# Kernel tuning notes

Measured on AMD Instinct MI355X. Metric: run time of the kernel, lower is better.

## Reference

```python
import jax, jax.numpy as jnp
import numpy as np

BLOCK = 128
SPARSE_BLOCK = 128
SF = 4
NEG = jnp.finfo(jnp.float32).min


def _unfold(x, size, step):
    # x: (..., T, d) -> (..., b, size, d) overlapping windows (torch unfold + transpose)
    b = (x.shape[-2] - size) // step + 1
    idx = np.arange(b)[:, None] * step + np.arange(size)
    return x[..., idx, :]


def _pad_tokens(x, s, pad_value):
    cfg = [(0, 0)] * (x.ndim - 2) + [(s, s), (0, 0)]
    return jnp.pad(x, cfg, constant_values=pad_value)


def _local_blocks(x, pad_value):
    size, step = BLOCK * 3, BLOCK
    s = (size - step) // 2
    return _unfold(_pad_tokens(x, s, pad_value), size, step)


def _sparse_blocks(x, pad_value):
    size0, step = SPARSE_BLOCK * 3, BLOCK // SF
    odd = step % 2
    size = size0 * 2
    s = (size - step) // 2 + odd
    xw = _unfold(_pad_tokens(x, s, pad_value), size, step)
    if odd:
        xw = xw[..., :-1, :, :]
    u = (size - BLOCK * 3 // SF) // 2 + odd
    sb = SPARSE_BLOCK
    u_ = u + odd
    return jnp.concatenate([xw[..., u - sb:u, :], xw[..., -u_:-u_ + sb, :]], axis=-2)


def _cat_gsl(x_global, x_sparse, x_local):
    # x_local: (n,h,b,t_loc,d); broadcast global over block axis
    b = x_local.shape[-3]
    g = jnp.broadcast_to(x_global[..., None, :, :],
                         x_global.shape[:-2] + (b,) + x_global.shape[-2:])
    return jnp.concatenate([g, x_sparse, x_local], axis=-2)


def _build_lsg(x, x_sparse, x_global, pad_value):
    loc = _local_blocks(x, pad_value)
    sp = _sparse_blocks(x_sparse, pad_value)
    return _cat_gsl(x_global, sp, loc)


def reference(query_layer, key_layer, value_layer, attention_mask,
              sparse_key, sparse_value, sparse_mask,
              global_key, global_value, global_mask):
    n, h, t, d = query_layer.shape
    n_blocks = t // BLOCK

    keys = _build_lsg(key_layer, sparse_key, global_key, 0.0)      # (n,h,b,K,d)
    vals = _build_lsg(value_layer, sparse_value, global_value, 0.0)

    # masks: (n,1,1,T) treated as d=1 token data after transpose
    m = jnp.swapaxes(attention_mask, -1, -2)    # (n,1,t,1)
    sm = jnp.swapaxes(sparse_mask, -1, -2)      # (n,1,t/SF,1)
    gm = jnp.swapaxes(global_mask, -1, -2)      # (n,1,g,1)
    mask = _build_lsg(m, sm, gm, NEG)           # (n,1,b,K,1)
    mask = jnp.swapaxes(mask, -1, -2)           # (n,1,b,1,K)

    q = query_layer.reshape(n, h, n_blocks, BLOCK, d)
    scores = jnp.einsum('nhbqd,nhbkd->nhbqk', q, keys) / jnp.sqrt(jnp.float32(d))
    probs = jax.nn.softmax(scores + mask, axis=-1)
    ctx = jnp.einsum('nhbqk,nhbkd->nhbqd', probs, vals)
    return ctx.reshape(n, h, t, d)


def setup_inputs() -> dict:
    key = jax.random.key(0)
    n, h, t, d = 2, 12, 4096, 64
    g = 64
    ts = t // SF
    k = jax.random.split(key, 7)
    return {
        'query_layer': jax.random.normal(k[0], (n, h, t, d), jnp.float32),
        'key_layer': jax.random.normal(k[1], (n, h, t, d), jnp.float32),
        'value_layer': jax.random.normal(k[2], (n, h, t, d), jnp.float32),
        'attention_mask': jnp.zeros((n, 1, 1, t), jnp.float32),
        'sparse_key': jax.random.normal(k[3], (n, h, ts, d), jnp.float32),
        'sparse_value': jax.random.normal(k[4], (n, h, ts, d), jnp.float32),
        'sparse_mask': jnp.zeros((n, 1, 1, ts), jnp.float32),
        'global_key': jax.random.normal(k[5], (n, h, g, d), jnp.float32),
        'global_value': jax.random.normal(k[6], (n, h, g, d), jnp.float32),
        'global_mask': jnp.zeros((n, 1, 1, g), jnp.float32),
    }
```

## Files before the change

### kernel.cpp

```cpp
#include <hip/hip_runtime.h>
#include <hip/hip_bf16.h>

typedef __attribute__((ext_vector_type(8))) short short8;
typedef __attribute__((ext_vector_type(4))) float f32x4;

#define LOG2E 1.44269504f
#define SCL2  0.18033688f
#define MNEG  -3.0e38f
#define MINIT -1.0e30f

__device__ __forceinline__ short f2bf(float f) {
  union { float f; unsigned u; } x; x.f = f;
  return (short)((x.u + 0x7FFFu + ((x.u >> 16) & 1u)) >> 16);
}
__device__ __forceinline__ float exp2g(float x) {
  float r; asm("v_exp_f32 %0, %1" : "=v"(r) : "v"(x)); return r;
}
__device__ __forceinline__ unsigned cvt_pk_bf16(float lo, float hi) {
  unsigned r;
  asm("v_cvt_pk_bf16_f32 %0, %1, %2" : "=v"(r) : "v"(lo), "v"(hi));
  return r;
}

__device__ __forceinline__ void conv_one(
    const float* __restrict__ src, short* __restrict__ dst,
    int Tin, int pad, int cid) {
  int Tpad = Tin + 2 * pad;
  int row = cid >> 3;
  int d0 = (cid & 7) * 8;
  int tok = row % Tpad;
  int nh = row / Tpad;
  int st = tok - pad;
  short8 o;
  if (st >= 0 && st < Tin) {
    const float4* sp = (const float4*)(src + ((size_t)nh * Tin + st) * 64 + d0);
    float4 f0 = sp[0], f1 = sp[1];
    o[0] = f2bf(f0.x); o[1] = f2bf(f0.y); o[2] = f2bf(f0.z); o[3] = f2bf(f0.w);
    o[4] = f2bf(f1.x); o[5] = f2bf(f1.y); o[6] = f2bf(f1.z); o[7] = f2bf(f1.w);
  } else {
#pragma unroll
    for (int j = 0; j < 8; ++j) o[j] = 0;
  }
  *(short8*)(dst + (size_t)row * 64 + d0) = o;
}

__device__ __forceinline__ void transv_one(
    const float* __restrict__ src, short* __restrict__ dst,
    int Tin, int pad, int tiles, int bidx, int tid, short (*lt)[72]) {
  int tile = bidx % tiles;
  int nh = bidx / tiles;
  int Tpad = Tin + 2 * pad;
  int c0 = tile * 64;
  int tok = tid >> 2;
  int dc = (tid & 3) * 16;
  int st = c0 + tok - pad;
  if (st >= 0 && st < Tin) {
    const float4* sp = (const float4*)(src + ((size_t)nh * Tin + st) * 64 + dc);
#pragma unroll
    for (int i = 0; i < 4; ++i) {
      float4 f = sp[i];
      lt[tok][dc + i * 4 + 0] = f2bf(f.x);
      lt[tok][dc + i * 4 + 1] = f2bf(f.y);
      lt[tok][dc + i * 4 + 2] = f2bf(f.z);
      lt[tok][dc + i * 4 + 3] = f2bf(f.w);
    }
  } else {
#pragma unroll
    for (int i = 0; i < 16; ++i) lt[tok][dc + i] = 0;
  }
  __syncthreads();
  int d = tid >> 2;
  int tc = (tid & 3) * 16;
  short8 o0, o1;
#pragma unroll
  for (int j = 0; j < 8; ++j) { o0[j] = lt[tc + j][d]; o1[j] = lt[tc + 8 + j][d]; }
  short* dp = dst + ((size_t)nh * 64 + d) * Tpad + c0 + tc;
  *(short8*)(dp) = o0;
  *(short8*)(dp + 8) = o1;
}

__global__ __launch_bounds__(256) void prepass_all(
    const float* __restrict__ K, const float* __restrict__ SK,
    const float* __restrict__ GK,
    const float* __restrict__ V, const float* __restrict__ SV,
    const float* __restrict__ GV,
    short* __restrict__ KL, short* __restrict__ KS, short* __restrict__ KG,
    short* __restrict__ VTL, short* __restrict__ VTS, short* __restrict__ VTG,
    const float* __restrict__ am, const float* __restrict__ sm,
    const float* __restrict__ gm,
    float* __restrict__ AM2, float* __restrict__ SM2, float* __restrict__ GM2) {
  __shared__ short lt[64][72];
  int bidx = blockIdx.x;
  int tid = threadIdx.x;
  if (bidx < 3264) { conv_one(K,  KL, 4096, 128, bidx * 256 + tid); return; }
  bidx -= 3264;
  if (bidx < 1008) { conv_one(SK, KS, 1024, 160, bidx * 256 + tid); return; }
  bidx -= 1008;
  if (bidx < 48)   { conv_one(GK, KG, 64, 0, bidx * 256 + tid); return; }
  bidx -= 48;
  if (bidx < 1632) { transv_one(V,  VTL, 4096, 128, 68, bidx, tid, lt); return; }
  bidx -= 1632;
  if (bidx < 504)  { transv_one(SV, VTS, 1024, 160, 21, bidx, tid, lt); return; }
  bidx -= 504;
  if (bidx < 24)   { transv_one(GV, VTG, 64, 0, 1, bidx, tid, lt); return; }
  bidx -= 24;
  int i = bidx * 256 + tid;
  if (i < 2 * 4352) {
    int n = i / 4352, rr = i % 4352, s = rr - 128;
    AM2[i] = (s >= 0 && s < 4096) ? am[n * 4096 + s] * LOG2E : MNEG;
  } else if (i < 2 * 4352 + 2 * 1344) {
    int j = i - 2 * 4352;
    int n = j / 1344, rr = j % 1344, s = rr - 160;
    SM2[j] = (s >= 0 && s < 1024) ? sm[n * 1024 + s] * LOG2E : MNEG;
  } else {
    int j = i - 2 * 4352 - 2 * 1344;
    GM2[j] = gm[j] * LOG2E;
  }
}

__global__ __launch_bounds__(512, 4) void lsg_attn8(
    const short* __restrict__ KL, const short* __restrict__ VTL,
    const short* __restrict__ KS, const short* __restrict__ VTS,
    const short* __restrict__ KG, const short* __restrict__ VTG,
    const float* __restrict__ AM2, const float* __restrict__ SM2,
    const float* __restrict__ GM2,
    const float* __restrict__ q_, float* __restrict__ out) {
  constexpr int TPL = 4352, TPS = 1344;
  __shared__ __align__(16) char smem[49152];

  int bid = blockIdx.x;
  bid = (bid & 7) * 96 + (bid >> 3);
  const int b = bid & 31, nh = bid >> 5, n_ = nh / 12;
  const int tid = threadIdx.x;
  const int wid = tid >> 6, lane = tid & 63;
  const int c = lane & 15, g = lane >> 4;
  const int r = tid >> 3, ch = tid & 7;
  const int skey = 4 * (r & 15) + (r >> 4);
  char* pbase = smem + 32768 + wid * 2048;
  const unsigned stg = ((unsigned)r << 7) + ((unsigned)(ch * 16) ^ ((unsigned)(r & 7) << 4));

  unsigned long long enc = 0; int nt = 0;
  {
    auto push = [&](int t) { enc |= (unsigned long long)t << (4 * nt); ++nt; };
    push(0);
    if (b >= 4)  push(1);
    if (b >= 2)  push(2);
    if (b <= 29) push(3);
    if (b <= 27) push(4);
    if (b >= 1)  { push(5); push(6); }
    push(7); push(8);
    if (b <= 30) { push(9); push(10); }
  }

  const float* qb = q_ + ((size_t)nh * 4096 + (size_t)b * 128 + wid * 16) * 64;
  short8 qa[2];
#pragma unroll
  for (int kc = 0; kc < 2; ++kc) {
    const float* qp = qb + (size_t)c * 64 + kc * 32 + g * 8;
    float4 f0 = *(const float4*)(qp);
    float4 f1 = *(const float4*)(qp + 4);
    short8 tq;
    tq[0] = f2bf(f0.x); tq[1] = f2bf(f0.y); tq[2] = f2bf(f0.z); tq[3] = f2bf(f0.w);
    tq[4] = f2bf(f1.x); tq[5] = f2bf(f1.y); tq[6] = f2bf(f1.z); tq[7] = f2bf(f1.w);
    qa[kc] = tq;
  }

  f32x4 acc[4];
  float mrun[4], lrun[4];
#pragma unroll
  for (int dd = 0; dd < 4; ++dd) acc[dd] = f32x4{0.f, 0.f, 0.f, 0.f};
#pragma unroll
  for (int j = 0; j < 4; ++j) { mrun[j] = MINIT; lrun[j] = 0.f; }

  auto src_for = [&](int t, const short*& kp, const short*& vp,
                     const float*& mp, int& stride) {
    if (t == 0) {
      kp = KG + (size_t)nh * (64 * 64);
      vp = VTG + (size_t)nh * (64 * 64);
      mp = GM2 + n_ * 64;
      stride = 64;
    } else if (t <= 4) {
      int r0 = b * 32 + (t - 1) * 64 + (t >= 3 ? 96 : 0);
      kp = KS + ((size_t)nh * TPS + r0) * 64;
      vp = VTS + (size_t)nh * (64 * TPS) + r0;
      mp = SM2 + n_ * TPS + r0;
      stride = TPS;
    } else {
      int r0 = b * 128 + (t - 5) * 64;
      kp = KL + ((size_t)nh * TPL + r0) * 64;
      vp = VTL + (size_t)nh * (64 * TPL) + r0;
      mp = AM2 + n_ * TPL + r0;
      stride = TPL;
    }
  };

  short8 kr, vr;
  float m_cur[4], m_nxt[4];

  {
    const short* kp; const short* vp; const float* mp; int st;
    src_for(0, kp, vp, mp, st);
    kr = *(const short8*)(kp + skey * 64 + ch * 8);
    vr = *(const short8*)(vp + (size_t)r * st + ch * 8);
#pragma unroll
    for (int i = 0; i < 4; ++i) m_cur[i] = mp[4 * c + i];
    *(short8*)(smem + stg) = kr;
    *(short8*)(smem + 16384 + stg) = vr;
    src_for((int)((enc >> 4) & 15ull), kp, vp, mp, st);
    kr = *(const short8*)(kp + skey * 64 + ch * 8);
    vr = *(const short8*)(vp + (size_t)r * st + ch * 8);
  }

  for (int i = 0; i < nt; ++i) {
    asm volatile("s_waitcnt lgkmcnt(0)\n\ts_barrier" ::: "memory");
    const int cur = i & 1, nxt = cur ^ 1;
    char* kbuf = smem + cur * 8192;
    char* vbuf = smem + 16384 + cur * 8192;

    short8 bk[4][2];
#pragma unroll
    for (int kt = 0; kt < 4; ++kt)
#pragma unroll
      for (int kc = 0; kc < 2; ++kc) {
        unsigned off = ((unsigned)(kt * 16 + c) << 7) +
                       ((unsigned)(kc * 64 + g * 16) ^ ((unsigned)(c & 7) << 4));
        bk[kt][kc] = *(const short8*)(kbuf + off);
      }

    if (i + 1 < nt) {
      *(short8*)(smem + nxt * 8192 + stg) = kr;
      *(short8*)(smem + 16384 + nxt * 8192 + stg) = vr;
    }
    if (i + 2 < nt) {
      int tn = (int)((enc >> (4 * (i + 2))) & 15ull);
      const short* kp; const short* vp; const float* mp; int st;
      src_for(tn, kp, vp, mp, st);
      kr = *(const short8*)(kp + skey * 64 + ch * 8);
      vr = *(const short8*)(vp + (size_t)r * st + ch * 8);
    }
    if (i + 1 < nt) {
      int tn = (int)((enc >> (4 * (i + 1))) & 15ull);
      const short* kp; const short* vp; const float* mp; int st;
      src_for(tn, kp, vp, mp, st);
#pragma unroll
      for (int j = 0; j < 4; ++j) m_nxt[j] = mp[4 * c + j];
    }

    f32x4 s4[4];
    __builtin_amdgcn_s_setprio(1);
#pragma unroll
    for (int kt = 0; kt < 4; ++kt) {
      f32x4 z = f32x4{0.f, 0.f, 0.f, 0.f};
      z = __builtin_amdgcn_mfma_f32_16x16x32_bf16(qa[0], bk[kt][0], z, 0, 0, 0);
      z = __builtin_amdgcn_mfma_f32_16x16x32_bf16(qa[1], bk[kt][1], z, 0, 0, 0);
      s4[kt] = z;
    }
    __builtin_amdgcn_s_setprio(0);
#pragma unroll
    for (int kt = 0; kt < 4; ++kt)
#pragma unroll
      for (int j = 0; j < 4; ++j)
        s4[kt][j] = fmaf(s4[kt][j], SCL2, m_cur[kt]);

    float rs[4];
    float worst = 0.f;
#pragma unroll
    for (int j = 0; j < 4; ++j) {
      float mo = mrun[j];
      float p0 = exp2g(s4[0][j] - mo);
      float p1 = exp2g(s4[1][j] - mo);
      float p2 = exp2g(s4[2][j] - mo);
      float p3 = exp2g(s4[3][j] - mo);
      rs[j] = (p0 + p1) + (p2 + p3);
      worst = fmaxf(worst, rs[j]);
      unsigned w0 = cvt_pk_bf16(p0, p1);
      unsigned w1 = cvt_pk_bf16(p2, p3);
      int row = 4 * g + j;
      unsigned bo = ((unsigned)row << 7) + ((unsigned)c << 3);
      bo ^= (unsigned)((row & 7) << 4);
      uint2 u; u.x = w0; u.y = w1;
      *(uint2*)(pbase + bo) = u;
    }

    if (__any(worst > 4096.f)) {
#pragma unroll
      for (int j = 0; j < 4; ++j) {
        float v0 = s4[0][j], v1 = s4[1][j];
        float v2 = s4[2][j], v3 = s4[3][j];
        float tv = fmaxf(fmaxf(v0, v1), fmaxf(v2, v3));
        tv = fmaxf(tv, __shfl_xor(tv, 1));
        tv = fmaxf(tv, __shfl_xor(tv, 2));
        tv = fmaxf(tv, __shfl_xor(tv, 4));
        tv = fmaxf(tv, __shfl_xor(tv, 8));
        float mo = mrun[j];
        float mn = fmaxf(mo, tv);
        float sc = exp2g(mo - mn);
#pragma unroll
        for (int dd = 0; dd < 4; ++dd) acc[dd][j] *= sc;
        float p0 = exp2g(v0 - mn), p1 = exp2g(v1 - mn);
        float p2 = exp2g(v2 - mn), p3 = exp2g(v3 - mn);
        lrun[j] = lrun[j] * sc + ((p0 + p1) + (p2 + p3));
        mrun[j] = mn;
        unsigned w0 = cvt_pk_bf16(p0, p1);
        unsigned w1 = cvt_pk_bf16(p2, p3);
        int row = 4 * g + j;
        unsigned bo = ((unsigned)row << 7) + ((unsigned)c << 3);
        bo ^= (unsigned)((row & 7) << 4);
        uint2 u; u.x = w0; u.y = w1;
        *(uint2*)(pbase + bo) = u;
      }
    } else {
#pragma unroll
      for (int j = 0; j < 4; ++j) lrun[j] += rs[j];
    }

#pragma unroll
    for (int kk = 0; kk < 2; ++kk) {
      unsigned bo = ((unsigned)c << 7) + (unsigned)(kk * 64 + g * 16);
      bo ^= (unsigned)((c & 7) << 4);
      short8 pa = *(const short8*)(pbase + bo);
      __builtin_amdgcn_s_setprio(1);
#pragma unroll
      for (int dd = 0; dd < 4; ++dd) {
        unsigned voff = ((unsigned)(dd * 16 + c) << 7) +
                        ((unsigned)(kk * 64 + g * 16) ^ ((unsigned)(c & 7) << 4));
        short8 bv = *(const short8*)(vbuf + voff);
        acc[dd] = __builtin_amdgcn_mfma_f32_16x16x32_bf16(pa, bv, acc[dd], 0, 0, 0);
      }
      __builtin_amdgcn_s_setprio(0);
    }
#pragma unroll
    for (int j = 0; j < 4; ++j) m_cur[j] = m_nxt[j];
  }

  float inv[4];
#pragma unroll
  for (int j = 0; j < 4; ++j) {
    float l = lrun[j];
    l += __shfl_xor(l, 1);
    l += __shfl_xor(l, 2);
    l += __shfl_xor(l, 4);
    l += __shfl_xor(l, 8);
    inv[j] = 1.f / l;
  }
  __syncthreads();
  float* fst = (float*)smem + wid * (16 * 68);
#pragma unroll
  for (int j = 0; j < 4; ++j)
#pragma unroll
    for (int dd = 0; dd < 4; ++dd)
      fst[(4 * g + j) * 68 + dd * 16 + c] = acc[dd][j] * inv[j];
  int rr = lane >> 2, cc = lane & 3;
  const float* fs = (float*)smem + wid * (16 * 68) + rr * 68 + cc * 16;
  float* op = out + ((size_t)nh * 4096 + (size_t)b * 128 + wid * 16 + rr) * 64 + cc * 16;
#pragma unroll
  for (int i = 0; i < 4; ++i)
    *(float4*)(op + i * 4) = *(const float4*)(fs + i * 4);
}

__global__ __launch_bounds__(256) void lsg_attn_fb(
    const float* __restrict__ q_,  const float* __restrict__ k_,
    const float* __restrict__ v_,  const float* __restrict__ amask,
    const float* __restrict__ sk,  const float* __restrict__ sv,
    const float* __restrict__ smk, const float* __restrict__ gk,
    const float* __restrict__ gv,  const float* __restrict__ gmk,
    float* __restrict__ out) {
  constexpr int T = 4096, D = 64, TS = 1024;
  constexpr float NEGF = -3.402823466e38f;
  __shared__ __align__(16) short k_lds[32][72];
  __shared__ __align__(16) short v_lds[64][40];
  __shared__ __align__(16) short p_lds[4][32][40];
  __shared__ float m_lds[32];
  const int bid = blockIdx.x;
  const int b = bid & 31, nh = bid >> 5, n_ = nh / 12;
  const int tid = threadIdx.x, wid = tid >> 6, lane = tid & 63;
  const int c = lane & 15, g = lane >> 4;
  const float* qb = q_ + ((size_t)nh * T + (size_t)b * 128) * D;
  const float* kb = k_ + (size_t)nh * T * D;
  const float* vb = v_ + (size_t)nh * T * D;
  const float* skb = sk + (size_t)nh * TS * D;
  const float* svb = sv + (size_t)nh * TS * D;
  const float* gkb = gk + (size_t)nh * 64 * D;
  const float* gvb = gv + (size_t)nh * 64 * D;
  const float* am = amask + (size_t)n_ * T;
  const float* sm = smk + (size_t)n_ * TS;
  const float* gm = gmk + (size_t)n_ * 64;
  short8 qa[2][2];
#pragma unroll
  for (int mt = 0; mt < 2; ++mt)
#pragma unroll
    for (int kc = 0; kc < 2; ++kc) {
      const float* qp = qb + (size_t)(wid * 32 + mt * 16 + c) * D + kc * 32 + g * 8;
      short8 t;
#pragma unroll
      for (int j = 0; j < 8; ++j) t[j] = f2bf(qp[j]);
      qa[mt][kc] = t;
    }
  f32x4 acc[2][4];
#pragma unroll
  for (int mt = 0; mt < 2; ++mt)
#pragma unroll
    for (int dd = 0; dd < 4; ++dd) acc[mt][dd] = f32x4{0.f, 0.f, 0.f, 0.f};
  float mrun[2][4], lrun[2][4];
#pragma unroll
  for (int mt = 0; mt < 2; ++mt)
#pragma unroll
    for (int j = 0; j < 4; ++j) { mrun[mt][j] = NEGF; lrun[mt][j] = 0.f; }
  const int key_local = tid >> 3;
  const int seg = tid & 7;
  const int d0 = seg * 8;
  for (int tile = 0; tile < 22; ++tile) {
    __syncthreads();
    {
      const int kk = tile * 32 + key_local;
      const float* ksrc; const float* vsrc; float mval; bool valid;
      if (kk < 64) {
        ksrc = gkb + kk * D; vsrc = gvb + kk * D; mval = gm[kk]; valid = true;
      } else if (kk < 320) {
        int s = b * 32 - 160 + (kk - 64) + ((kk >= 192) ? 96 : 0);
        valid = (s >= 0) && (s < TS);
        int sc2 = valid ? s : 0;
        ksrc = skb + sc2 * D; vsrc = svb + sc2 * D;
        mval = valid ? sm[sc2] : NEGF;
      } else {
        int tt = b * 128 - 128 + (kk - 320);
        valid = (tt >= 0) && (tt < T);
        int tc = valid ? tt : 0;
        ksrc = kb + tc * D; vsrc = vb + tc * D;
        mval = valid ? am[tc] : NEGF;
      }
      short8 k8; short v8[8];
      if (valid) {
#pragma unroll
        for (int j = 0; j < 8; ++j) { k8[j] = f2bf(ksrc[d0 + j]); v8[j] = f2bf(vsrc[d0 + j]); }
      } else {
#pragma unroll
        for (int j = 0; j < 8; ++j) { k8[j] = 0; v8[j] = 0; }
      }
      *(short8*)(&k_lds[key_local][d0]) = k8;
#pragma unroll
      for (int j = 0; j < 8; ++j) v_lds[d0 + j][key_local] = v8[j];
      if (seg == 0) m_lds[key_local] = mval;
    }
    __syncthreads();
    short8 bk[2][2];
#pragma unroll
    for (int kt = 0; kt < 2; ++kt)
#pragma unroll
      for (int kc = 0; kc < 2; ++kc)
        bk[kt][kc] = *(const short8*)(&k_lds[kt * 16 + c][kc * 32 + g * 8]);
    f32x4 s_[2][2];
#pragma unroll
    for (int mt = 0; mt < 2; ++mt)
#pragma unroll
      for (int kt = 0; kt < 2; ++kt) {
        f32x4 z = f32x4{0.f, 0.f, 0.f, 0.f};
        z = __builtin_amdgcn_mfma_f32_16x16x32_bf16(qa[mt][0], bk[kt][0], z, 0, 0, 0);
        z = __builtin_amdgcn_mfma_f32_16x16x32_bf16(qa[mt][1], bk[kt][1], z, 0, 0, 0);
        s_[mt][kt] = z;
      }
    const float msk0 = m_lds[c];
    const float msk1 = m_lds[16 + c];
#pragma unroll
    for (int mt = 0; mt < 2; ++mt) {
#pragma unroll
      for (int j = 0; j < 4; ++j) {
        float s0 = s_[mt][0][j] * 0.125f + msk0;
        float s1 = s_[mt][1][j] * 0.125f + msk1;
        float tv = fmaxf(s0, s1);
        tv = fmaxf(tv, __shfl_xor(tv, 1));
        tv = fmaxf(tv, __shfl_xor(tv, 2));
        tv = fmaxf(tv, __shfl_xor(tv, 4));
        tv = fmaxf(tv, __shfl_xor(tv, 8));
        float mold = mrun[mt][j];
        float mnew = fmaxf(mold, tv);
        float scale = __expf(mold - mnew);
        mrun[mt][j] = mnew;
        float p0 = __expf(s0 - mnew);
        float p1 = __expf(s1 - mnew);
        lrun[mt][j] = lrun[mt][j] * scale + p0 + p1;
#pragma unroll
        for (int dd = 0; dd < 4; ++dd) acc[mt][dd][j] *= scale;
        p_lds[wid][mt * 16 + g * 4 + j][c] = f2bf(p0);
        p_lds[wid][mt * 16 + g * 4 + j][16 + c] = f2bf(p1);
      }
    }
    __syncthreads();
#pragma unroll
    for (int mt = 0; mt < 2; ++mt) {
      short8 pa = *(const short8*)(&p_lds[wid][mt * 16 + c][g * 8]);
#pragma unroll
      for (int dd = 0; dd < 4; ++dd) {
        short8 bv = *(const short8*)(&v_lds[dd * 16 + c][g * 8]);
        acc[mt][dd] = __builtin_amdgcn_mfma_f32_16x16x32_bf16(pa, bv, acc[mt][dd], 0, 0, 0);
      }
    }
  }
  float* ob = out + ((size_t)nh * T + (size_t)b * 128 + (size_t)wid * 32) * D;
#pragma unroll
  for (int mt = 0; mt < 2; ++mt)
#pragma unroll
    for (int j = 0; j < 4; ++j) {
      float l = lrun[mt][j];
      l += __shfl_xor(l, 1);
      l += __shfl_xor(l, 2);
      l += __shfl_xor(l, 4);
      l += __shfl_xor(l, 8);
      float inv = 1.f / l;
      int row = mt * 16 + g * 4 + j;
#pragma unroll
      for (int dd = 0; dd < 4; ++dd)
        ob[(size_t)row * D + dd * 16 + c] = acc[mt][dd][j] * inv;
    }
}

extern "C" void kernel_launch(void* const* d_in, const int* in_sizes, int n_in,
                              void* d_out, int out_size, void* d_ws, size_t ws_size,
                              hipStream_t stream) {
  const float* q  = (const float*)d_in[0];
  const float* k  = (const float*)d_in[1];
  const float* v  = (const float*)d_in[2];
  const float* am = (const float*)d_in[3];
  const float* sk = (const float*)d_in[4];
  const float* sv = (const float*)d_in[5];
  const float* sm = (const float*)d_in[6];
  const float* gk = (const float*)d_in[7];
  const float* gv = (const float*)d_in[8];
  const float* gm = (const float*)d_in[9];
  float* out = (float*)d_out;

  size_t off = 0;
  char* base = (char*)d_ws;
  auto alloc = [&](size_t bytes) { void* p = base + off; off += bytes; return p; };
  short* KL  = (short*)alloc(13369344);
  short* VTL = (short*)alloc(13369344);
  short* KS  = (short*)alloc(4128768);
  short* VTS = (short*)alloc(4128768);
  short* KG  = (short*)alloc(196608);
  short* VTG = (short*)alloc(196608);
  float* AM2 = (float*)alloc(34816);
  float* SM2 = (float*)alloc(10752);
  float* GM2 = (float*)alloc(512);

  if (off <= ws_size) {
    hipLaunchKernelGGL(prepass_all, dim3(6525), dim3(256), 0, stream,
                       k, sk, gk, v, sv, gv, KL, KS, KG, VTL, VTS, VTG,
                       am, sm, gm, AM2, SM2, GM2);
    hipLaunchKernelGGL(lsg_attn8, dim3(768), dim3(512), 0, stream,
                       KL, VTL, KS, VTS, KG, VTG, AM2, SM2, GM2, q, out);
  } else {
    hipLaunchKernelGGL(lsg_attn_fb, dim3(768), dim3(256), 0, stream,
                       q, k, v, am, sk, sv, sm, gk, gv, gm, out);
  }
}
```

Before: 58.56 us.

## Swap QK^T MFMA operands so probabilities feed PV MFMA directly from registers

Computes S^T by swapping the MFMA operands and permutes the K row staging order, so each lane holds the probabilities in exactly the layout the PV MFMA A-operand needs. This removes the per-wave LDS round trip for P (write, then read back), shrinks shared memory, and turns the per-row max and sum reductions into two cross-group shuffles. Rescale factors are passed through a small LDS scratch area, and masks are loaded as vectors each iteration instead of being prefetched one step ahead.

```diff
diff --git a/kernel.cpp b/kernel.cpp
--- a/kernel.cpp
+++ b/kernel.cpp
@@ -3,6 +3,7 @@
 
 typedef __attribute__((ext_vector_type(8))) short short8;
 typedef __attribute__((ext_vector_type(4))) float f32x4;
+typedef __attribute__((ext_vector_type(4))) unsigned u32x4;
 
 #define LOG2E 1.44269504f
 #define SCL2  0.18033688f
@@ -118,7 +119,7 @@
   }
 }
 
-__global__ __launch_bounds__(512, 4) void lsg_attn8(
+__global__ __launch_bounds__(512, 4) void lsg_attn9(
     const short* __restrict__ KL, const short* __restrict__ VTL,
     const short* __restrict__ KS, const short* __restrict__ VTS,
     const short* __restrict__ KG, const short* __restrict__ VTG,
@@ -126,7 +127,7 @@
     const float* __restrict__ GM2,
     const float* __restrict__ q_, float* __restrict__ out) {
   constexpr int TPL = 4352, TPS = 1344;
-  __shared__ __align__(16) char smem[49152];
+  __shared__ __align__(16) char smem[35328];
 
   int bid = blockIdx.x;
   bid = (bid & 7) * 96 + (bid >> 3);
@@ -135,8 +136,9 @@
   const int wid = tid >> 6, lane = tid & 63;
   const int c = lane & 15, g = lane >> 4;
   const int r = tid >> 3, ch = tid & 7;
-  const int skey = 4 * (r & 15) + (r >> 4);
-  char* pbase = smem + 32768 + wid * 2048;
+  const int skey = ((r >> 5) << 5) | (((r >> 2) & 3) << 3) |
+                   (((r >> 4) & 1) << 2) | (r & 3);
+  float* sclw = (float*)(smem + 32768) + wid * 16;
   const unsigned stg = ((unsigned)r << 7) + ((unsigned)(ch * 16) ^ ((unsigned)(r & 7) << 4));
 
   unsigned long long enc = 0; int nt = 0;
@@ -166,11 +168,9 @@
   }
 
   f32x4 acc[4];
-  float mrun[4], lrun[4];
 #pragma unroll
   for (int dd = 0; dd < 4; ++dd) acc[dd] = f32x4{0.f, 0.f, 0.f, 0.f};
-#pragma unroll
-  for (int j = 0; j < 4; ++j) { mrun[j] = MINIT; lrun[j] = 0.f; }
+  float mrun = MINIT, lrun = 0.f;
 
   auto src_for = [&](int t, const short*& kp, const short*& vp,
                      const float*& mp, int& stride) {
@@ -195,15 +195,12 @@
   };
 
   short8 kr, vr;
-  float m_cur[4], m_nxt[4];
 
   {
     const short* kp; const short* vp; const float* mp; int st;
     src_for(0, kp, vp, mp, st);
     kr = *(const short8*)(kp + skey * 64 + ch * 8);
     vr = *(const short8*)(vp + (size_t)r * st + ch * 8);
-#pragma unroll
-    for (int i = 0; i < 4; ++i) m_cur[i] = mp[4 * c + i];
     *(short8*)(smem + stg) = kr;
     *(short8*)(smem + 16384 + stg) = vr;
     src_for((int)((enc >> 4) & 15ull), kp, vp, mp, st);
@@ -216,6 +213,16 @@
     const int cur = i & 1, nxt = cur ^ 1;
     char* kbuf = smem + cur * 8192;
     char* vbuf = smem + 16384 + cur * 8192;
+
+    f32x4 mk[4];
+    {
+      int tl = (int)((enc >> (4 * i)) & 15ull);
+      const short* kp; const short* vp; const float* mp; int st;
+      src_for(tl, kp, vp, mp, st);
+#pragma unroll
+      for (int kt = 0; kt < 4; ++kt)
+        mk[kt] = *(const f32x4*)(mp + ((kt >> 1) << 5) + g * 8 + ((kt & 1) << 2));
+    }
 
     short8 bk[4][2];
 #pragma unroll
@@ -238,21 +245,14 @@
       kr = *(const short8*)(kp + skey * 64 + ch * 8);
       vr = *(const short8*)(vp + (size_t)r * st + ch * 8);
     }
-    if (i + 1 < nt) {
-      int tn = (int)((enc >> (4 * (i + 1))) & 15ull);
-      const short* kp; const short* vp; const float* mp; int st;
-      src_for(tn, kp, vp, mp, st);
-#pragma unroll
-      for (int j = 0; j < 4; ++j) m_nxt[j] = mp[4 * c + j];
-    }
 
     f32x4 s4[4];
     __builtin_amdgcn_s_setprio(1);
 #pragma unroll
     for (int kt = 0; kt < 4; ++kt) {
       f32x4 z = f32x4{0.f, 0.f, 0.f, 0.f};
-      z = __builtin_amdgcn_mfma_f32_16x16x32_bf16(qa[0], bk[kt][0], z, 0, 0, 0);
-      z = __builtin_amdgcn_mfma_f32_16x16x32_bf16(qa[1], bk[kt][1], z, 0, 0, 0);
+      z = __builtin_amdgcn_mfma_f32_16x16x32_bf16(bk[kt][0], qa[0], z, 0, 0, 0);
+      z = __builtin_amdgcn_mfma_f32_16x16x32_bf16(bk[kt][1], qa[1], z, 0, 0, 0);
       s4[kt] = z;
     }
     __builtin_amdgcn_s_setprio(0);
@@ -260,65 +260,58 @@
     for (int kt = 0; kt < 4; ++kt)
 #pragma unroll
       for (int j = 0; j < 4; ++j)
-        s4[kt][j] = fmaf(s4[kt][j], SCL2, m_cur[kt]);
-
-    float rs[4];
-    float worst = 0.f;
-#pragma unroll
-    for (int j = 0; j < 4; ++j) {
-      float mo = mrun[j];
-      float p0 = exp2g(s4[0][j] - mo);
-      float p1 = exp2g(s4[1][j] - mo);
-      float p2 = exp2g(s4[2][j] - mo);
-      float p3 = exp2g(s4[3][j] - mo);
-      rs[j] = (p0 + p1) + (p2 + p3);
-      worst = fmaxf(worst, rs[j]);
-      unsigned w0 = cvt_pk_bf16(p0, p1);
-      unsigned w1 = cvt_pk_bf16(p2, p3);
-      int row = 4 * g + j;
-      unsigned bo = ((unsigned)row << 7) + ((unsigned)c << 3);
-      bo ^= (unsigned)((row & 7) << 4);
-      uint2 u; u.x = w0; u.y = w1;
-      *(uint2*)(pbase + bo) = u;
-    }
-
-    if (__any(worst > 4096.f)) {
+        s4[kt][j] = fmaf(s4[kt][j], SCL2, mk[kt][j]);
+
+    float rs = 0.f;
+    f32x4 p4[4];
+#pragma unroll
+    for (int kt = 0; kt < 4; ++kt)
 #pragma unroll
       for (int j = 0; j < 4; ++j) {
-        float v0 = s4[0][j], v1 = s4[1][j];
-        float v2 = s4[2][j], v3 = s4[3][j];
-        float tv = fmaxf(fmaxf(v0, v1), fmaxf(v2, v3));
-        tv = fmaxf(tv, __shfl_xor(tv, 1));
-        tv = fmaxf(tv, __shfl_xor(tv, 2));
-        tv = fmaxf(tv, __shfl_xor(tv, 4));
-        tv = fmaxf(tv, __shfl_xor(tv, 8));
-        float mo = mrun[j];
-        float mn = fmaxf(mo, tv);
-        float sc = exp2g(mo - mn);
-#pragma unroll
-        for (int dd = 0; dd < 4; ++dd) acc[dd][j] *= sc;
-        float p0 = exp2g(v0 - mn), p1 = exp2g(v1 - mn);
-        float p2 = exp2g(v2 - mn), p3 = exp2g(v3 - mn);
-        lrun[j] = lrun[j] * sc + ((p0 + p1) + (p2 + p3));
-        mrun[j] = mn;
-        unsigned w0 = cvt_pk_bf16(p0, p1);
-        unsigned w1 = cvt_pk_bf16(p2, p3);
-        int row = 4 * g + j;
-        unsigned bo = ((unsigned)row << 7) + ((unsigned)c << 3);
-        bo ^= (unsigned)((row & 7) << 4);
-        uint2 u; u.x = w0; u.y = w1;
-        *(uint2*)(pbase + bo) = u;
-      }
+        float p = exp2g(s4[kt][j] - mrun);
+        p4[kt][j] = p;
+        rs += p;
+      }
+
+    if (__any(rs > 4096.f)) {
+      float tv = s4[0][0];
+#pragma unroll
+      for (int kt = 0; kt < 4; ++kt)
+#pragma unroll
+        for (int j = 0; j < 4; ++j) tv = fmaxf(tv, s4[kt][j]);
+      tv = fmaxf(tv, __shfl_xor(tv, 16));
+      tv = fmaxf(tv, __shfl_xor(tv, 32));
+      float mn = fmaxf(mrun, tv);
+      float sc = exp2g(mrun - mn);
+      if (lane < 16) sclw[lane] = sc;
+      rs = 0.f;
+#pragma unroll
+      for (int kt = 0; kt < 4; ++kt)
+#pragma unroll
+        for (int j = 0; j < 4; ++j) {
+          float p = exp2g(s4[kt][j] - mn);
+          p4[kt][j] = p;
+          rs += p;
+        }
+      lrun = lrun * sc + rs;
+      mrun = mn;
+      f32x4 sq = *(const f32x4*)&sclw[4 * g];
+#pragma unroll
+      for (int dd = 0; dd < 4; ++dd)
+#pragma unroll
+        for (int j = 0; j < 4; ++j) acc[dd][j] *= sq[j];
     } else {
-#pragma unroll
-      for (int j = 0; j < 4; ++j) lrun[j] += rs[j];
+      lrun += rs;
     }
 
 #pragma unroll
     for (int kk = 0; kk < 2; ++kk) {
-      unsigned bo = ((unsigned)c << 7) + (unsigned)(kk * 64 + g * 16);
-      bo ^= (unsigned)((c & 7) << 4);
-      short8 pa = *(const short8*)(pbase + bo);
+      u32x4 uu;
+      uu[0] = cvt_pk_bf16(p4[2 * kk][0], p4[2 * kk][1]);
+      uu[1] = cvt_pk_bf16(p4[2 * kk][2], p4[2 * kk][3]);
+      uu[2] = cvt_pk_bf16(p4[2 * kk + 1][0], p4[2 * kk + 1][1]);
+      uu[3] = cvt_pk_bf16(p4[2 * kk + 1][2], p4[2 * kk + 1][3]);
+      short8 pa = __builtin_bit_cast(short8, uu);
       __builtin_amdgcn_s_setprio(1);
 #pragma unroll
       for (int dd = 0; dd < 4; ++dd) {
@@ -329,27 +322,20 @@
       }
       __builtin_amdgcn_s_setprio(0);
     }
-#pragma unroll
-    for (int j = 0; j < 4; ++j) m_cur[j] = m_nxt[j];
-  }
-
-  float inv[4];
-#pragma unroll
-  for (int j = 0; j < 4; ++j) {
-    float l = lrun[j];
-    l += __shfl_xor(l, 1);
-    l += __shfl_xor(l, 2);
-    l += __shfl_xor(l, 4);
-    l += __shfl_xor(l, 8);
-    inv[j] = 1.f / l;
-  }
+  }
+
+  float l = lrun;
+  l += __shfl_xor(l, 16);
+  l += __shfl_xor(l, 32);
+  if (lane < 16) sclw[lane] = 1.f / l;
+  f32x4 iv = *(const f32x4*)&sclw[4 * g];
   __syncthreads();
   float* fst = (float*)smem + wid * (16 * 68);
 #pragma unroll
   for (int j = 0; j < 4; ++j)
 #pragma unroll
     for (int dd = 0; dd < 4; ++dd)
-      fst[(4 * g + j) * 68 + dd * 16 + c] = acc[dd][j] * inv[j];
+      fst[(4 * g + j) * 68 + dd * 16 + c] = acc[dd][j] * iv[j];
   int rr = lane >> 2, cc = lane & 3;
   const float* fs = (float*)smem + wid * (16 * 68) + rr * 68 + cc * 16;
   float* op = out + ((size_t)nh * 4096 + (size_t)b * 128 + wid * 16 + rr) * 64 + cc * 16;
@@ -546,7 +532,7 @@
     hipLaunchKernelGGL(prepass_all, dim3(6525), dim3(256), 0, stream,
                        k, sk, gk, v, sv, gv, KL, KS, KG, VTL, VTS, VTG,
                        am, sm, gm, AM2, SM2, GM2);
-    hipLaunchKernelGGL(lsg_attn8, dim3(768), dim3(512), 0, stream,
+    hipLaunchKernelGGL(lsg_attn9, dim3(768), dim3(512), 0, stream,
                        KL, VTL, KS, VTS, KG, VTG, AM2, SM2, GM2, q, out);
   } else {
     hipLaunchKernelGGL(lsg_attn_fb, dim3(768), dim3(256), 0, stream,
```

Result: no change. 58.74 us (+0.3%).
